# Kernel tuning notes

Measured on AMD Instinct MI355X. Metric: run time of the kernel, lower is better.

The kernel has to match this reference:

```python
import jax, jax.numpy as jnp
import numpy as np

EPS = 1e-8

def _ternary(weight):
    # scale = mean(|W|); quantize to {-1,0,1}*scale with straight-through estimator
    scale = jnp.abs(weight).mean()
    w_norm = weight / jnp.maximum(scale, EPS)
    q = jnp.clip(jnp.round(w_norm), -1.0, 1.0) * scale
    # STE: forward value is q, gradient flows to `weight` as identity
    return weight + jax.lax.stop_gradient(q - weight)

def setup_inputs() -> dict:
    key = jax.random.key(0)
    k1, k2, k3 = jax.random.split(key, 3)
    B, S, D_IN, D_OUT = 8, 8192, 1024, 1024
    x = jax.random.normal(k1, (B, S, D_IN), dtype=jnp.float32)
    weight = jax.random.normal(k2, (D_OUT, D_IN), dtype=jnp.float32) * 0.02
    bias = jax.random.normal(k3, (D_OUT,), dtype=jnp.float32) * 0.01
    return {"x": x, "weight": weight, "bias": bias}

def reference(x, weight, bias):
    w_t = _ternary(weight)  # [out, in]
    # F.linear: x @ W^T + b
    return jnp.einsum('bsi,oi->bso', x, w_t) + bias
```

## Files before the change

kernel.cpp:

```cpp
#include <hip/hip_runtime.h>
#include <stdint.h>
#include <stddef.h>

typedef __bf16 bf16_t;
typedef __bf16 bf16x8 __attribute__((ext_vector_type(8)));
typedef __bf16 bf16x4 __attribute__((ext_vector_type(4)));
typedef float  f32x4  __attribute__((ext_vector_type(4)));

__global__ __launch_bounds__(256)
void k_abssum(const float* __restrict__ W, float* __restrict__ partials) {
    const int t = threadIdx.x;
    const int b = blockIdx.x;
    const f32x4* W4 = reinterpret_cast<const f32x4*>(W);
    float s = 0.f;
    const int base = b * 1024 + t;
#pragma unroll
    for (int i = 0; i < 4; ++i) {
        f32x4 v = W4[base + i * 256];
        s += fabsf(v[0]) + fabsf(v[1]) + fabsf(v[2]) + fabsf(v[3]);
    }
#pragma unroll
    for (int off = 32; off > 0; off >>= 1) s += __shfl_down(s, off);
    __shared__ float red[4];
    if ((t & 63) == 0) red[t >> 6] = s;
    __syncthreads();
    if (t == 0) partials[b] = red[0] + red[1] + red[2] + red[3];
}

__global__ __launch_bounds__(256)
void k_ternarize(const float* __restrict__ W, const float* __restrict__ partials,
                 bf16_t* __restrict__ T, float* __restrict__ scale_out) {
    const int t = threadIdx.x;
    const int b = blockIdx.x;
    float s = partials[t];
#pragma unroll
    for (int off = 32; off > 0; off >>= 1) s += __shfl_down(s, off);
    __shared__ float red[4];
    if ((t & 63) == 0) red[t >> 6] = s;
    __syncthreads();
    const float total = red[0] + red[1] + red[2] + red[3];
    const float scale = total * (1.0f / 1048576.0f);
    const float inv   = 1.0f / fmaxf(scale, 1e-8f);

    const int idx = b * 256 + t;
    f32x4 w = reinterpret_cast<const f32x4*>(W)[idx];
    bf16x4 q;
#pragma unroll
    for (int j = 0; j < 4; ++j) {
        float qn = rintf(w[j] * inv);
        qn = fminf(1.f, fmaxf(-1.f, qn));
        q[j] = (bf16_t)qn;
    }
    reinterpret_cast<bf16x4*>(T)[idx] = q;
    if (b == 0 && t == 0) scale_out[0] = scale;
}

__global__ __launch_bounds__(256)
void k_gemm(const float* __restrict__ X, const bf16_t* __restrict__ T,
            const float* __restrict__ bias, const float* __restrict__ scale_p,
            float* __restrict__ Out) {
    __shared__ bf16_t As[128][40];
    __shared__ bf16_t Bs[128][32];

    const int tid  = threadIdx.x;
    const int lane = tid & 63;
    const int w    = tid >> 6;
    const int wr   = w >> 1;
    const int wc   = w & 1;

    const int bid = blockIdx.x;
    const int sid = (bid & 7) * 512 + (bid >> 3);
    const int bn  = sid & 7;
    const int bm  = sid >> 3;
    const int row0 = bm * 128;
    const int col0 = bn * 128;

    const int ar = tid >> 2;
    const int ac = (tid & 3) * 8;
    const float* xA0 = X + (size_t)(row0 + ar) * 1024 + ac;
    const float* xA1 = X + (size_t)(row0 + ar + 64) * 1024 + ac;

    const int brow = w * 32 + (lane >> 2);
    const int bcol = (lane & 3) * 8;
    const bf16_t* gB = T + (size_t)(col0 + brow) * 1024 + bcol;

    f32x4 acc[4][4];
    {
        f32x4 z = {0.f, 0.f, 0.f, 0.f};
#pragma unroll
        for (int i = 0; i < 4; ++i)
#pragma unroll
            for (int j = 0; j < 4; ++j) acc[i][j] = z;
    }

    f32x4 a_reg[2][2];
#define LOAD_A(kt)                                                             \
    {                                                                          \
        const float* p0 = xA0 + (kt) * 32;                                     \
        const float* p1 = xA1 + (kt) * 32;                                     \
        a_reg[0][0] = *(const f32x4*)(p0);                                     \
        a_reg[0][1] = *(const f32x4*)(p0 + 4);                                 \
        a_reg[1][0] = *(const f32x4*)(p1);                                     \
        a_reg[1][1] = *(const f32x4*)(p1 + 4);                                 \
    }

    LOAD_A(0);

    const int g16 = (lane >> 4) * 8;
    const int rl  = lane & 15;

    for (int kt = 0; kt < 32; ++kt) {
        __syncthreads();
#pragma unroll
        for (int h = 0; h < 2; ++h) {
            bf16x8 v;
#pragma unroll
            for (int j = 0; j < 4; ++j) {
                v[j]     = (bf16_t)a_reg[h][0][j];
                v[4 + j] = (bf16_t)a_reg[h][1][j];
            }
            *reinterpret_cast<bf16x8*>(&As[ar + h * 64][ac]) = v;
        }
        {
            const bf16_t* g0 = gB + kt * 32;
            __builtin_amdgcn_global_load_lds(
                (const __attribute__((address_space(1))) void*)g0,
                (__attribute__((address_space(3))) void*)&Bs[w * 32][0], 16, 0, 0);
            __builtin_amdgcn_global_load_lds(
                (const __attribute__((address_space(1))) void*)(g0 + 16 * 1024),
                (__attribute__((address_space(3))) void*)&Bs[w * 32 + 16][0], 16, 0, 0);
        }
        __syncthreads();

        if (kt + 1 < 32) LOAD_A(kt + 1);

        bf16x8 af[4], bfr[4];
#pragma unroll
        for (int mi = 0; mi < 4; ++mi)
            af[mi] = *reinterpret_cast<const bf16x8*>(&As[wr * 64 + mi * 16 + rl][g16]);
#pragma unroll
        for (int ni = 0; ni < 4; ++ni)
            bfr[ni] = *reinterpret_cast<const bf16x8*>(&Bs[wc * 64 + ni * 16 + rl][g16]);
#pragma unroll
        for (int mi = 0; mi < 4; ++mi)
#pragma unroll
            for (int ni = 0; ni < 4; ++ni)
                acc[mi][ni] = __builtin_amdgcn_mfma_f32_16x16x32_bf16(
                    af[mi], bfr[ni], acc[mi][ni], 0, 0, 0);
    }

    const float scale = scale_p[0];
    float bv[4];
#pragma unroll
    for (int ni = 0; ni < 4; ++ni)
        bv[ni] = bias[col0 + wc * 64 + ni * 16 + rl];
#pragma unroll
    for (int mi = 0; mi < 4; ++mi) {
        const int gm0 = row0 + wr * 64 + mi * 16 + (lane >> 4) * 4;
#pragma unroll
        for (int ni = 0; ni < 4; ++ni) {
            const int gn = col0 + wc * 64 + ni * 16 + rl;
#pragma unroll
            for (int j = 0; j < 4; ++j)
                Out[(size_t)(gm0 + j) * 1024 + gn] = acc[mi][ni][j] * scale + bv[ni];
        }
    }
#undef LOAD_A
}

extern "C" void kernel_launch(void* const* d_in, const int* in_sizes, int n_in,
                              void* d_out, int out_size, void* d_ws, size_t ws_size,
                              hipStream_t stream) {
    const float* x    = (const float*)d_in[0];
    const float* W    = (const float*)d_in[1];
    const float* bias = (const float*)d_in[2];
    float* out = (float*)d_out;

    float*  ws_part  = (float*)d_ws;
    float*  ws_scale = ws_part + 256;
    bf16_t* ws_T     = (bf16_t*)(ws_part + 512);

    hipLaunchKernelGGL(k_abssum,    dim3(256),  dim3(256), 0, stream, W, ws_part);
    hipLaunchKernelGGL(k_ternarize, dim3(1024), dim3(256), 0, stream, W, ws_part, ws_T, ws_scale);
    hipLaunchKernelGGL(k_gemm,      dim3(4096), dim3(256), 0, stream, x, ws_T, bias, ws_scale, out);
}
```

Measured before the change: 612.6 us.

## Deepen GEMM K-tile to 64 with pre-tiled weight layout and swizzled LDS

The ternarize kernel now writes the quantized weights in a blocked layout that matches the GEMM's 128x64 B tiles, so each K step loads B into LDS with contiguous global_load_lds transfers. The GEMM K tile grows from 32 to 64, which halves the barrier iterations and doubles the MFMA work between syncs. The A tile is stored with an XOR-style row swizzle to avoid LDS bank conflicts. LDS per block grows to 32KB and a launch-bounds hint of 3 blocks per CU is added, which may limit occupancy or registers.

After: 576.1 us. -6.0%, faster.

```diff
diff --git a/kernel.cpp b/kernel.cpp
--- a/kernel.cpp
+++ b/kernel.cpp
@@ -31,7 +31,6 @@
 void k_ternarize(const float* __restrict__ W, const float* __restrict__ partials,
                  bf16_t* __restrict__ T, float* __restrict__ scale_out) {
     const int t = threadIdx.x;
-    const int b = blockIdx.x;
     float s = partials[t];
 #pragma unroll
     for (int off = 32; off > 0; off >>= 1) s += __shfl_down(s, off);
@@ -42,47 +41,73 @@
     const float scale = total * (1.0f / 1048576.0f);
     const float inv   = 1.0f / fmaxf(scale, 1e-8f);
 
-    const int idx = b * 256 + t;
-    f32x4 w = reinterpret_cast<const f32x4*>(W)[idx];
-    bf16x4 q;
+    const int c  = blockIdx.x * 256 + t;
+    const int n  = c >> 7;
+    const int k  = (c & 127) * 8;
+    const float* wp = W + (size_t)n * 1024 + k;
+    f32x4 w0 = *reinterpret_cast<const f32x4*>(wp);
+    f32x4 w1 = *reinterpret_cast<const f32x4*>(wp + 4);
+    bf16x8 q;
 #pragma unroll
     for (int j = 0; j < 4; ++j) {
-        float qn = rintf(w[j] * inv);
-        qn = fminf(1.f, fmaxf(-1.f, qn));
-        q[j] = (bf16_t)qn;
-    }
-    reinterpret_cast<bf16x4*>(T)[idx] = q;
-    if (b == 0 && t == 0) scale_out[0] = scale;
-}
-
-__global__ __launch_bounds__(256)
+        float q0 = fminf(1.f, fmaxf(-1.f, rintf(w0[j] * inv)));
+        float q1 = fminf(1.f, fmaxf(-1.f, rintf(w1[j] * inv)));
+        q[j]     = (bf16_t)q0;
+        q[4 + j] = (bf16_t)q1;
+    }
+    const int bn = n >> 7, nn = n & 127;
+    const int kt = k >> 6, kq8 = (k & 63) >> 3;
+    const size_t chunk = ((size_t)(bn * 16 + kt) * 8 + kq8) * 128 + nn;
+    reinterpret_cast<bf16x8*>(T)[chunk] = q;
+    if (c == 0) scale_out[0] = scale;
+}
+
+__global__ __launch_bounds__(256, 3)
 void k_gemm(const float* __restrict__ X, const bf16_t* __restrict__ T,
             const float* __restrict__ bias, const float* __restrict__ scale_p,
             float* __restrict__ Out) {
-    __shared__ bf16_t As[128][40];
-    __shared__ bf16_t Bs[128][32];
+    __shared__ bf16_t As[8192];
+    __shared__ bf16_t Bs[8192];
 
     const int tid  = threadIdx.x;
     const int lane = tid & 63;
     const int w    = tid >> 6;
     const int wr   = w >> 1;
     const int wc   = w & 1;
-
-    const int bid = blockIdx.x;
-    const int sid = (bid & 7) * 512 + (bid >> 3);
-    const int bn  = sid & 7;
-    const int bm  = sid >> 3;
+    const int lq   = lane >> 4;
+    const int rl   = lane & 15;
+
+    const int bid  = blockIdx.x;
+    const int sid  = (bid & 7) * 512 + (bid >> 3);
+    const int bn   = sid & 7;
+    const int bm   = sid >> 3;
     const int row0 = bm * 128;
     const int col0 = bn * 128;
 
-    const int ar = tid >> 2;
-    const int ac = (tid & 3) * 8;
-    const float* xA0 = X + (size_t)(row0 + ar) * 1024 + ac;
-    const float* xA1 = X + (size_t)(row0 + ar + 64) * 1024 + ac;
-
-    const int brow = w * 32 + (lane >> 2);
-    const int bcol = (lane & 3) * 8;
-    const bf16_t* gB = T + (size_t)(col0 + brow) * 1024 + bcol;
+    const int am  = tid >> 3;
+    const int akq = tid & 7;
+    const float* xA = X + (size_t)(row0 + am) * 1024 + akq * 8;
+    int awoff[4];
+#pragma unroll
+    for (int h = 0; h < 4; ++h) {
+        const int m = am + 32 * h;
+        awoff[h] = (akq * 128 + (m & ~7) + ((m + akq) & 7)) * 16;
+    }
+
+    const bf16_t* gB = T + (size_t)bn * 16 * 8192 + (size_t)(w * 4) * 512 + (size_t)lane * 8;
+    bf16_t* ldsB = Bs + (size_t)(w * 4) * 512;
+
+    int aoff[2][4], boff[2][4];
+#pragma unroll
+    for (int kk = 0; kk < 2; ++kk) {
+        const int kq8 = kk * 4 + lq;
+#pragma unroll
+        for (int i = 0; i < 4; ++i) {
+            const int m = wr * 64 + i * 16 + rl;
+            aoff[kk][i] = (kq8 * 128 + (m & ~7) + ((m + kq8) & 7)) * 16;
+            boff[kk][i] = (kq8 * 128 + wc * 64 + i * 16 + rl) * 16;
+        }
+    }
 
     f32x4 acc[4][4];
     {
@@ -93,60 +118,55 @@
             for (int j = 0; j < 4; ++j) acc[i][j] = z;
     }
 
-    f32x4 a_reg[2][2];
-#define LOAD_A(kt)                                                             \
-    {                                                                          \
-        const float* p0 = xA0 + (kt) * 32;                                     \
-        const float* p1 = xA1 + (kt) * 32;                                     \
-        a_reg[0][0] = *(const f32x4*)(p0);                                     \
-        a_reg[0][1] = *(const f32x4*)(p0 + 4);                                 \
-        a_reg[1][0] = *(const f32x4*)(p1);                                     \
-        a_reg[1][1] = *(const f32x4*)(p1 + 4);                                 \
+    f32x4 a0[4], a1[4];
+#define LOAD_A(kt)                                                          \
+    {                                                                       \
+        _Pragma("unroll")                                                   \
+        for (int h = 0; h < 4; ++h) {                                       \
+            const float* p = xA + (size_t)h * 32 * 1024 + (kt) * 64;        \
+            a0[h] = *(const f32x4*)(p);                                     \
+            a1[h] = *(const f32x4*)(p + 4);                                 \
+        }                                                                   \
     }
 
     LOAD_A(0);
 
-    const int g16 = (lane >> 4) * 8;
-    const int rl  = lane & 15;
-
-    for (int kt = 0; kt < 32; ++kt) {
+    for (int kt = 0; kt < 16; ++kt) {
         __syncthreads();
 #pragma unroll
-        for (int h = 0; h < 2; ++h) {
+        for (int i = 0; i < 4; ++i)
+            __builtin_amdgcn_global_load_lds(
+                (const __attribute__((address_space(1))) void*)(gB + (size_t)kt * 8192 + i * 512),
+                (__attribute__((address_space(3))) void*)(ldsB + i * 512), 16, 0, 0);
+#pragma unroll
+        for (int h = 0; h < 4; ++h) {
             bf16x8 v;
 #pragma unroll
             for (int j = 0; j < 4; ++j) {
-                v[j]     = (bf16_t)a_reg[h][0][j];
-                v[4 + j] = (bf16_t)a_reg[h][1][j];
+                v[j]     = (bf16_t)a0[h][j];
+                v[4 + j] = (bf16_t)a1[h][j];
             }
-            *reinterpret_cast<bf16x8*>(&As[ar + h * 64][ac]) = v;
-        }
-        {
-            const bf16_t* g0 = gB + kt * 32;
-            __builtin_amdgcn_global_load_lds(
-                (const __attribute__((address_space(1))) void*)g0,
-                (__attribute__((address_space(3))) void*)&Bs[w * 32][0], 16, 0, 0);
-            __builtin_amdgcn_global_load_lds(
-                (const __attribute__((address_space(1))) void*)(g0 + 16 * 1024),
-                (__attribute__((address_space(3))) void*)&Bs[w * 32 + 16][0], 16, 0, 0);
+            *reinterpret_cast<bf16x8*>((char*)As + awoff[h]) = v;
         }
         __syncthreads();
 
-        if (kt + 1 < 32) LOAD_A(kt + 1);
-
-        bf16x8 af[4], bfr[4];
-#pragma unroll
-        for (int mi = 0; mi < 4; ++mi)
-            af[mi] = *reinterpret_cast<const bf16x8*>(&As[wr * 64 + mi * 16 + rl][g16]);
-#pragma unroll
-        for (int ni = 0; ni < 4; ++ni)
-            bfr[ni] = *reinterpret_cast<const bf16x8*>(&Bs[wc * 64 + ni * 16 + rl][g16]);
-#pragma unroll
-        for (int mi = 0; mi < 4; ++mi)
-#pragma unroll
-            for (int ni = 0; ni < 4; ++ni)
-                acc[mi][ni] = __builtin_amdgcn_mfma_f32_16x16x32_bf16(
-                    af[mi], bfr[ni], acc[mi][ni], 0, 0, 0);
+        if (kt + 1 < 16) LOAD_A(kt + 1);
+
+#pragma unroll
+        for (int kk = 0; kk < 2; ++kk) {
+            bf16x8 af[4], bfr[4];
+#pragma unroll
+            for (int i = 0; i < 4; ++i) {
+                af[i]  = *reinterpret_cast<const bf16x8*>((const char*)As + aoff[kk][i]);
+                bfr[i] = *reinterpret_cast<const bf16x8*>((const char*)Bs + boff[kk][i]);
+            }
+#pragma unroll
+            for (int mi = 0; mi < 4; ++mi)
+#pragma unroll
+                for (int ni = 0; ni < 4; ++ni)
+                    acc[mi][ni] = __builtin_amdgcn_mfma_f32_16x16x32_bf16(
+                        af[mi], bfr[ni], acc[mi][ni], 0, 0, 0);
+        }
     }
 
     const float scale = scale_p[0];
@@ -156,7 +176,7 @@
         bv[ni] = bias[col0 + wc * 64 + ni * 16 + rl];
 #pragma unroll
     for (int mi = 0; mi < 4; ++mi) {
-        const int gm0 = row0 + wr * 64 + mi * 16 + (lane >> 4) * 4;
+        const int gm0 = row0 + wr * 64 + mi * 16 + lq * 4;
 #pragma unroll
         for (int ni = 0; ni < 4; ++ni) {
             const int gn = col0 + wc * 64 + ni * 16 + rl;
@@ -180,7 +200,7 @@
     float*  ws_scale = ws_part + 256;
     bf16_t* ws_T     = (bf16_t*)(ws_part + 512);
 
-    hipLaunchKernelGGL(k_abssum,    dim3(256),  dim3(256), 0, stream, W, ws_part);
-    hipLaunchKernelGGL(k_ternarize, dim3(1024), dim3(256), 0, stream, W, ws_part, ws_T, ws_scale);
+    hipLaunchKernelGGL(k_abssum,    dim3(256), dim3(256), 0, stream, W, ws_part);
+    hipLaunchKernelGGL(k_ternarize, dim3(512), dim3(256), 0, stream, W, ws_part, ws_T, ws_scale);
     hipLaunchKernelGGL(k_gemm,      dim3(4096), dim3(256), 0, stream, x, ws_T, bias, ws_scale, out);
 }
```
